# Performance work log

Hardware: AMD Instinct MI355X
Metric: run time of the kernel (lower is better)

Reference implementation:

```python
import jax, jax.numpy as jnp
import numpy as np

T, B, E, H, DFF, K = 1024, 4, 512, 8, 2048, 31
D = E // H  # head_dim


def double_swish(x):
    # DoubleSwish: x * sigmoid(x - 1)
    return x * jax.nn.sigmoid(x - 1.0)


def ffn(x, w1, b1, w2, b2):
    # ScaledLinear -> ActivationBalancer(identity in eval) -> DoubleSwish -> ScaledLinear
    return double_swish(x @ w1.T + b1) @ w2.T + b2


def rel_shift(x):
    # x: (B, H, T, 2T-1) -> (B, H, T, T); out[b,h,i,j] = x[b,h,i, (T-1) - i + j]
    t = x.shape[2]
    idx = (t - 1) - jnp.arange(t)[:, None] + jnp.arange(t)[None, :]  # (T, T)
    return jnp.take_along_axis(x, idx[None, None], axis=-1)


def self_attn(x, pos_emb, wqkv, bqkv, wo, bo, wpos, u, v):
    # x: (T, B, E); Transformer-XL style rel-pos multi-head attention
    t, b, e = x.shape
    qkv = x @ wqkv.T + bqkv                       # (T, B, 3E)
    q, k, val = jnp.split(qkv, 3, axis=-1)
    q = q * (D ** -0.5)
    to_heads = lambda z: z.reshape(t, b, H, D).transpose(1, 2, 0, 3)  # (B,H,T,D)
    q, k, val = to_heads(q), to_heads(k), to_heads(val)
    # positional projection: (1, 2T-1, E) -> (1, H, D, 2T-1)
    p = (pos_emb @ wpos.T).reshape(1, 2 * t - 1, H, D).transpose(0, 2, 3, 1)
    ac = jnp.einsum('bhld,bhsd->bhls', q + u[None, :, None, :], k)
    bd = jnp.einsum('bhld,bhdm->bhlm', q + v[None, :, None, :], p)
    scores = ac + rel_shift(bd)                   # (B, H, T, T)
    attn = jax.nn.softmax(scores, axis=-1)
    out = jnp.einsum('bhls,bhsd->bhld', attn, val)
    out = out.transpose(2, 0, 1, 3).reshape(t, b, e)  # (T, B, E)
    return out @ wo.T + bo


def conv_module(x, pw1_w, pw1_b, dw_w, dw_b, pw2_w, pw2_b):
    # x: (T, B, C) -> (B, C, T)
    x = x.transpose(1, 2, 0)
    x = jnp.einsum('oc,bct->bot', pw1_w, x) + pw1_b[None, :, None]  # (B, 2C, T)
    a, g = jnp.split(x, 2, axis=1)
    x = a * jax.nn.sigmoid(g)                     # GLU over channel dim
    pad = (K - 1) // 2
    x = jax.lax.conv_general_dilated(
        x, dw_w, window_strides=(1,), padding=[(pad, pad)],
        dimension_numbers=('NCH', 'OIH', 'NCH'), feature_group_count=E)
    x = double_swish(x + dw_b[None, :, None])
    x = jnp.einsum('oc,bct->bot', pw2_w, x) + pw2_b[None, :, None]
    return x.transpose(2, 0, 1)                   # (T, B, C)


def basic_norm(x, log_eps):
    # BasicNorm: x * (mean(x^2, -1) + exp(eps))^{-0.5}
    return x * jax.lax.rsqrt(jnp.mean(x * x, axis=-1, keepdims=True) + jnp.exp(log_eps))


def setup_inputs() -> dict:
    key = jax.random.key(0)
    ks = jax.random.split(key, 24)
    std = jnp.float32(0.02)
    f = lambda k, s: jax.random.normal(k, s, jnp.float32)
    return dict(
        src=f(ks[0], (T, B, E)),
        pos_emb=f(ks[1], (1, 2 * T - 1, E)),
        in_proj_w=f(ks[2], (3 * E, E)) * std,
        in_proj_b=f(ks[3], (3 * E,)) * std,
        out_proj_w=f(ks[4], (E, E)) * std,
        out_proj_b=f(ks[5], (E,)) * std,
        linear_pos_w=f(ks[6], (E, E)) * std,
        pos_bias_u=f(ks[7], (H, D)) * jnp.float32(0.01),
        pos_bias_v=f(ks[8], (H, D)) * jnp.float32(0.01),
        ffm_w1=f(ks[9], (DFF, E)) * std, ffm_b1=f(ks[10], (DFF,)) * std,
        ffm_w2=f(ks[11], (E, DFF)) * std, ffm_b2=f(ks[12], (E,)) * std,
        ff_w1=f(ks[13], (DFF, E)) * std, ff_b1=f(ks[14], (DFF,)) * std,
        ff_w2=f(ks[15], (E, DFF)) * std, ff_b2=f(ks[16], (E,)) * std,
        conv_pw1_w=f(ks[17], (2 * E, E)) * std, conv_pw1_b=f(ks[18], (2 * E,)) * std,
        conv_dw_w=f(ks[19], (E, 1, K)) * std, conv_dw_b=f(ks[20], (E,)) * std,
        conv_pw2_w=f(ks[21], (E, E)) * std, conv_pw2_b=f(ks[22], (E,)) * std,
        norm_eps=jnp.array(np.log(0.25), jnp.float32),
    )


def reference(src, pos_emb, in_proj_w, in_proj_b, out_proj_w, out_proj_b,
              linear_pos_w, pos_bias_u, pos_bias_v,
              ffm_w1, ffm_b1, ffm_w2, ffm_b2,
              ff_w1, ff_b1, ff_w2, ff_b2,
              conv_pw1_w, conv_pw1_b, conv_dw_w, conv_dw_b, conv_pw2_w, conv_pw2_b,
              norm_eps):
    # macaron FFN
    x = src + ffn(src, ffm_w1, ffm_b1, ffm_w2, ffm_b2)
    # rel-pos self-attention
    x = x + self_attn(x, pos_emb, in_proj_w, in_proj_b, out_proj_w, out_proj_b,
                      linear_pos_w, pos_bias_u, pos_bias_v)
    # convolution module
    x = x + conv_module(x, conv_pw1_w, conv_pw1_b, conv_dw_w, conv_dw_b, conv_pw2_w, conv_pw2_b)
    # second FFN
    x = x + ffn(x, ff_w1, ff_b1, ff_w2, ff_b2)
    # balancer is identity in eval; final BasicNorm
    return basic_norm(x, norm_eps)
```

## Files before the change

kernel.cpp:

```cpp
#include <hip/hip_runtime.h>
#include <string.h>


#define T_ 1024
#define B_ 4
#define E_ 512
#define H_ 8
#define DFF_ 2048
#define KW_ 31

typedef unsigned short u16;
typedef unsigned int u32;
typedef __bf16 bf16x8 __attribute__((ext_vector_type(8)));
typedef float floatx4 __attribute__((ext_vector_type(4)));

__device__ __forceinline__ float b2f(u16 u) {
    return __uint_as_float(((u32)u) << 16);
}
__device__ __forceinline__ u16 f2b(float f) {
    u32 i = __float_as_uint(f);
    u32 r = (i + 0x7fffu + ((i >> 16) & 1u)) >> 16;
    return (u16)r;
}

__device__ __forceinline__ void glds16(const u16 *g, u16 *l) {
    __builtin_amdgcn_global_load_lds((const __attribute__((address_space(1))) void *)g,
                                     (__attribute__((address_space(3))) void *)l, 16, 0, 0);
}

__global__ __launch_bounds__(256) void fill_k(float *out, long long n, float val) {
    long long g = (long long)blockIdx.x * 256 + threadIdx.x;
    if (g < n) out[g] = val;
}

__global__ __launch_bounds__(256) void detect_k(const u16 *src16, int *flag) {
    __shared__ int sh[256];
    int tid = threadIdx.x;
    int cnt = 0;
    for (int i = tid; i < 4096; i += 256) {
        u16 x = src16[2 * i];
        int e = (x >> 7) & 0xFF;
        cnt += (e == 0 || (e >= 0x70 && e <= 0x8F)) ? 1 : 0;
    }
    sh[tid] = cnt;
    __syncthreads();
    for (int s = 128; s; s >>= 1) {
        if (tid < s) sh[tid] += sh[tid + s];
        __syncthreads();
    }
    if (tid == 0) *flag = (sh[0] < 2048) ? 1 : 0;
}

struct CVT {
    const void *in[24];
    long long pre[25];
};

__global__ __launch_bounds__(256) void convert_k(CVT c, u16 *dst, const int *flag,
                                                 long long total) {
    long long g = (long long)blockIdx.x * 256 + threadIdx.x;
    if (g >= total) return;
    int s = 0;
#pragma unroll
    for (int i = 1; i < 25; i++) s += (g >= c.pre[i]) ? 1 : 0;
    long long l = g - c.pre[s];
    int f = *flag;
    u16 v = f ? f2b(((const float *)c.in[s])[l]) : ((const u16 *)c.in[s])[l];
    dst[g] = v;
}

struct GP {
    const u16 *A, *B;
    u16 *C;
    const u16 *bias;
    const void *resin;
    float *xr;
    u16 *xb;
    const u16 *ub, *vb;
    u16 *qu, *qv, *kh, *vt;
    int M, N, K, lda, ldb, ldc, mode, qcols, resin_f32;
    float qscale;
};

__global__ __launch_bounds__(512) void gemm_nt(GP p) {
    __shared__ __align__(16) u16 As[3 * 4096];
    __shared__ __align__(16) u16 Bs[3 * 4096];
    const int tid = threadIdx.x;
    const int wv = tid >> 6, ln = tid & 63;
    const int l16 = ln & 15, quad = ln >> 4;
    const int wm = (wv >> 2) << 5;
    const int wn = (wv & 3) << 4;
    const int gx = gridDim.x;
    const int nb = gx * gridDim.y;
    const int lid = blockIdx.y * gx + blockIdx.x;
    const int nid = (lid & 7) * (nb >> 3) + (lid >> 3);
    const int m0 = (nid / gx) << 6, n0 = (nid % gx) << 6;
    floatx4 zero = {0.f, 0.f, 0.f, 0.f};
    floatx4 acc[2];
    acc[0] = zero;
    acc[1] = zero;

    const int NT = p.K >> 6;

    const int srow = tid >> 3;
    const int sg = ((tid & 7) ^ (srow & 7)) << 3;
    int ra = m0 + srow;
    if (ra > p.M - 1) ra = p.M - 1;
    const u16 *Agp = p.A + (long long)ra * p.lda + sg;
    const u16 *Bgp = p.B + (long long)(n0 + srow) * p.ldb + sg;

    auto stage = [&](int bidx, int t) {
        const int k0 = t << 6;
        const int o = bidx << 12;
        glds16(Agp + k0, As + o + tid * 8);
        glds16(Bgp + k0, Bs + o + tid * 8);
    };

    stage(0, 0);
    stage(1, 1);
    stage(2, 2);
    asm volatile("s_waitcnt vmcnt(4)" ::: "memory");
    __builtin_amdgcn_s_barrier();

    int cb = 0;
    for (int t = 0; t < NT; t++) {
        const int o = cb << 12;
#pragma unroll
        for (int kk = 0; kk < 2; kk++) {
            const int swz = ((((kk << 2) | quad) ^ (l16 & 7)) << 3);
            bf16x8 bfv = __builtin_bit_cast(bf16x8,
                *(const uint4 *)&Bs[o + ((wn + l16) << 6) + swz]);
#pragma unroll
            for (int mt = 0; mt < 2; mt++) {
                bf16x8 af = __builtin_bit_cast(bf16x8,
                    *(const uint4 *)&As[o + ((wm + (mt << 4) + l16) << 6) + swz]);
                acc[mt] = __builtin_amdgcn_mfma_f32_16x16x32_bf16(af, bfv, acc[mt], 0, 0, 0);
            }
        }
        if (t + 1 < NT) {
            __builtin_amdgcn_sched_barrier(0);
            __builtin_amdgcn_s_barrier();
            if (t + 3 < NT) {
                stage(cb, t + 3);
                asm volatile("s_waitcnt vmcnt(4)" ::: "memory");
            } else if (t + 2 < NT) {
                asm volatile("s_waitcnt vmcnt(2)" ::: "memory");
            } else {
                asm volatile("s_waitcnt vmcnt(0)" ::: "memory");
            }
            __builtin_amdgcn_s_barrier();
            __builtin_amdgcn_sched_barrier(0);
        }
        cb = (cb == 2) ? 0 : cb + 1;
    }

#pragma unroll
    for (int mt = 0; mt < 2; mt++) {
#pragma unroll
        for (int r = 0; r < 4; r++) {
            int gr = m0 + wm + (mt << 4) + (quad << 2) + r;
            int gc = n0 + wn + l16;
            bool oob = gr >= p.M;
            if (oob && p.mode != 3) continue;
            float y = 0.f;
            if (!oob) {
                y = acc[mt][r];
                if (p.bias) y += b2f(p.bias[gc]);
                if (gc < p.qcols) y *= p.qscale;
            }
            if (p.mode == 3) {
                p.C[((gc >> 6) << 17) + (gr << 6) + (gc & 63)] = f2b(y);
            } else if (p.mode == 0) {
                p.C[(long long)gr * p.ldc + gc] = f2b(y);
            } else if (p.mode == 1) {
                float s = 1.f / (1.f + __expf(1.f - y));
                p.C[(long long)gr * p.ldc + gc] = f2b(y * s);
            } else {
                long long idx = (long long)gr * p.ldc + gc;
                float rv = p.resin_f32 ? ((const float *)p.resin)[idx]
                                       : b2f(((const u16 *)p.resin)[idx]);
                float o = rv + y;
                p.xr[idx] = o;
                if (p.xb) p.xb[idx] = f2b(o);
            }
        }
    }
}

__global__ __launch_bounds__(512) void gemm_nt128(GP p) {
    __shared__ __align__(16) u16 As[3 * 4096];
    __shared__ __align__(16) u16 Bs[3 * 4096];
    const int tid = threadIdx.x;
    const int wv = tid >> 6, ln = tid & 63;
    const int l16 = ln & 15, quad = ln >> 4;
    const int wm = (wv >> 2) << 6;
    const int wn = (wv & 3) << 5;
    const int gx = gridDim.x;
    const int nb = gx * gridDim.y;
    const int lid = blockIdx.y * gx + blockIdx.x;
    const int nid = (lid & 7) * (nb >> 3) + (lid >> 3);
    const int m0 = (nid / gx) << 7, n0 = (nid % gx) << 7;
    const int srow = tid >> 2;
    const int sg = ((tid & 3) ^ ((tid >> 3) & 3)) << 3;
    const u16 *Agp = p.A + (long long)(m0 + srow) * p.lda + sg;
    const u16 *Bgp = p.B + (long long)(n0 + srow) * p.ldb + sg;
    floatx4 zero = {0.f, 0.f, 0.f, 0.f};
    floatx4 acc[4][2];
#pragma unroll
    for (int i = 0; i < 4; i++)
#pragma unroll
        for (int j = 0; j < 2; j++) acc[i][j] = zero;

    const int rswz = ((quad ^ ((l16 >> 1) & 3)) << 3);
    const int NT = p.K >> 5;

    auto stage = [&](int bidx, int t) {
        const int k0 = t << 5;
        const int o = bidx << 12;
        glds16(Agp + k0, As + o + tid * 8);
        glds16(Bgp + k0, Bs + o + tid * 8);
    };

    stage(0, 0);
    stage(1, 1);
    stage(2, 2);
    asm volatile("s_waitcnt vmcnt(4)" ::: "memory");
    __builtin_amdgcn_s_barrier();

    int cb = 0;
    for (int t = 0; t < NT; t++) {
        const int o = cb << 12;
        bf16x8 av[4], bv[2];
#pragma unroll
        for (int mt = 0; mt < 4; mt++)
            av[mt] = __builtin_bit_cast(bf16x8,
                *(const uint4 *)&As[o + ((wm + (mt << 4) + l16) << 5) + rswz]);
#pragma unroll
        for (int nt = 0; nt < 2; nt++)
            bv[nt] = __builtin_bit_cast(bf16x8,
                *(const uint4 *)&Bs[o + ((wn + (nt << 4) + l16) << 5) + rswz]);
#pragma unroll
        for (int mt = 0; mt < 4; mt++)
#pragma unroll
            for (int nt = 0; nt < 2; nt++)
                acc[mt][nt] = __builtin_amdgcn_mfma_f32_16x16x32_bf16(av[mt], bv[nt],
                                                                      acc[mt][nt], 0, 0, 0);
        if (t + 1 < NT) {
            __builtin_amdgcn_sched_barrier(0);
            __builtin_amdgcn_s_barrier();
            if (t + 3 < NT) {
                stage(cb, t + 3);
                asm volatile("s_waitcnt vmcnt(4)" ::: "memory");
            } else if (t + 2 < NT) {
                asm volatile("s_waitcnt vmcnt(2)" ::: "memory");
            } else {
                asm volatile("s_waitcnt vmcnt(0)" ::: "memory");
            }
            __builtin_amdgcn_s_barrier();
            __builtin_amdgcn_sched_barrier(0);
        }
        cb = (cb == 2) ? 0 : cb + 1;
    }

#pragma unroll
    for (int mt = 0; mt < 4; mt++)
#pragma unroll
        for (int nt = 0; nt < 2; nt++)
#pragma unroll
            for (int r = 0; r < 4; r++) {
                int gr = m0 + wm + (mt << 4) + (quad << 2) + r;
                int gc = n0 + wn + (nt << 4) + l16;
                float y = acc[mt][nt][r];
                if (p.bias) y += b2f(p.bias[gc]);
                if (gc < p.qcols) y *= p.qscale;
                if (p.mode == 0) {
                    p.C[(long long)gr * p.ldc + gc] = f2b(y);
                } else if (p.mode == 1) {
                    float s = 1.f / (1.f + __expf(1.f - y));
                    p.C[(long long)gr * p.ldc + gc] = f2b(y * s);
                } else if (p.mode == 4) {
                    int t = gr >> 2, b = gr & 3;
                    if (gc < E_) {
                        int z = b * 8 + (gc >> 6);
                        long long oq = ((long long)z << 16) + (t << 6) + (gc & 63);
                        p.qu[oq] = f2b(y + b2f(p.ub[gc]));
                        p.qv[oq] = f2b(y + b2f(p.vb[gc]));
                    } else if (gc < 2 * E_) {
                        int c = gc - E_;
                        int z = b * 8 + (c >> 6);
                        p.kh[((long long)z << 16) + (t << 6) + (c & 63)] = f2b(y);
                    } else {
                        int c = gc - 2 * E_;
                        int z = b * 8 + (c >> 6);
                        p.vt[(long long)((z << 6) + (c & 63)) * T_ + t] = f2b(y);
                    }
                } else {
                    long long idx = (long long)gr * p.ldc + gc;
                    float rv = p.resin_f32 ? ((const float *)p.resin)[idx]
                                           : b2f(((const u16 *)p.resin)[idx]);
                    float o = rv + y;
                    p.xr[idx] = o;
                    if (p.xb) p.xb[idx] = f2b(o);
                }
            }
}

__global__ __launch_bounds__(256) void gemm_glu(const u16 *A, const u16 *W, const u16 *bias,
                                                u16 *ch) {
    __shared__ __align__(16) u16 As[3 * 4096];
    __shared__ __align__(16) u16 Ba[3 * 4096];
    __shared__ __align__(16) u16 Bg[3 * 4096];
    const int tid = threadIdx.x;
    const int wv = tid >> 6, ln = tid & 63;
    const int l16 = ln & 15, quad = ln >> 4;
    const int gx = gridDim.x;
    const int nb = gx * gridDim.y;
    const int lid = blockIdx.y * gx + blockIdx.x;
    const int nid = (lid & 7) * (nb >> 3) + (lid >> 3);
    const int m0 = (nid / gx) << 6, n0 = (nid % gx) << 6;
    floatx4 zero = {0.f, 0.f, 0.f, 0.f};
    floatx4 aa[4], ag[4];
#pragma unroll
    for (int i = 0; i < 4; i++) { aa[i] = zero; ag[i] = zero; }

    const int NT = 8;

    auto stage = [&](int bidx, int t) {
        const int k0 = t << 6;
        const int o = bidx << 12;
#pragma unroll
        for (int ps = 0; ps < 2; ps++) {
            int g = ps * 256 + tid;
            int row = g >> 3;
            int src = ((g & 7) ^ (row & 7)) << 3;
            glds16(A + ((m0 + row) << 9) + k0 + src, As + o + g * 8);
            glds16(W + ((n0 + row) << 9) + k0 + src, Ba + o + g * 8);
            glds16(W + ((E_ + n0 + row) << 9) + k0 + src, Bg + o + g * 8);
        }
    };

    stage(0, 0);
    stage(1, 1);
    stage(2, 2);
    asm volatile("s_waitcnt vmcnt(12)" ::: "memory");
    __builtin_amdgcn_s_barrier();

    int cb = 0;
    for (int t = 0; t < NT; t++) {
        const int o = cb << 12;
#pragma unroll
        for (int kk = 0; kk < 2; kk++) {
            const int swz = ((((kk << 2) | quad) ^ (l16 & 7)) << 3);
            bf16x8 af = __builtin_bit_cast(bf16x8,
                *(const uint4 *)&As[o + (((wv << 4) | l16) << 6) + swz]);
#pragma unroll
            for (int nt = 0; nt < 4; nt++) {
                bf16x8 bfa = __builtin_bit_cast(bf16x8,
                    *(const uint4 *)&Ba[o + (((nt << 4) | l16) << 6) + swz]);
                aa[nt] = __builtin_amdgcn_mfma_f32_16x16x32_bf16(af, bfa, aa[nt], 0, 0, 0);
                bf16x8 bfg = __builtin_bit_cast(bf16x8,
                    *(const uint4 *)&Bg[o + (((nt << 4) | l16) << 6) + swz]);
                ag[nt] = __builtin_amdgcn_mfma_f32_16x16x32_bf16(af, bfg, ag[nt], 0, 0, 0);
            }
        }
        if (t + 1 < NT) {
            __builtin_amdgcn_sched_barrier(0);
            __builtin_amdgcn_s_barrier();
            if (t + 3 < NT) {
                stage(cb, t + 3);
                asm volatile("s_waitcnt vmcnt(12)" ::: "memory");
            } else if (t + 2 < NT) {
                asm volatile("s_waitcnt vmcnt(6)" ::: "memory");
            } else {
                asm volatile("s_waitcnt vmcnt(0)" ::: "memory");
            }
            __builtin_amdgcn_s_barrier();
            __builtin_amdgcn_sched_barrier(0);
        }
        cb = (cb == 2) ? 0 : cb + 1;
    }

#pragma unroll
    for (int nt = 0; nt < 4; nt++) {
#pragma unroll
        for (int r = 0; r < 4; r++) {
            int gr = m0 + (wv << 4) + (quad << 2) + r;
            int gc = n0 + (nt << 4) + l16;
            float a = aa[nt][r] + b2f(bias[gc]);
            float g = ag[nt][r] + b2f(bias[E_ + gc]);
            ch[((long long)gr << 9) + gc] = f2b(a * (1.f / (1.f + __expf(-g))));
        }
    }
}

struct FK {
    const u16 *QU, *QV, *KH, *PPH, *VT;
    u16 *attno;
};

__global__ __launch_bounds__(256) void flash_k(FK p) {
    __shared__ __align__(16) u16 lds[2 * 16384 + 4608];

    const int tid = threadIdx.x;
    const int wv = tid >> 6, ln = tid & 63;
    const int l16 = ln & 15, quad = ln >> 4;
    const int lid = blockIdx.y * 16 + blockIdx.x;
    const int nid = (lid & 7) * 64 + (lid >> 3);
    const int zg = nid >> 4;
    const int i0 = (nid & 15) << 6;
    const u16 *kh0 = p.KH + (long long)zg * 65536;
    const u16 *ph0 = p.PPH + (long long)(zg & 7) * 131072;
    const u16 *vt0 = p.VT + (long long)zg * 65536;
    u16 *Pb = lds + 32768;

    auto stage = [&](int buf, int jt) {
        const int j0 = jt << 6;
        const int m_start = 960 - i0 + j0;
        u16 *Kh = lds + (buf << 14);
        u16 *Vt = Kh + 4096;
        u16 *Ph = Kh + 8192;
#pragma unroll
        for (int ps = 0; ps < 2; ps++) {
            int g = ps * 256 + tid;
            int row = g >> 3;
            int src = ((g & 7) ^ (row & 7)) << 3;
            glds16(kh0 + ((j0 + row) << 6) + src, Kh + g * 8);
            glds16(vt0 + (row << 10) + j0 + src, Vt + g * 8);
        }
#pragma unroll
        for (int ps = 0; ps < 4; ps++) {
            int g = ps * 256 + tid;
            int row = g >> 3;
            int src = ((g & 7) ^ (row & 7)) << 3;
            glds16(ph0 + ((m_start + row) << 6) + src, Ph + g * 8);
        }
    };

    const long long qoff = (long long)zg * 65536 + (long long)(i0 + (wv << 4) + l16) * 64 + (quad << 3);
    bf16x8 aqu[2], aqv[2];
#pragma unroll
    for (int kk = 0; kk < 2; kk++) {
        aqu[kk] = __builtin_bit_cast(bf16x8, *(const uint4 *)(p.QU + qoff + (kk << 5)));
        aqv[kk] = __builtin_bit_cast(bf16x8, *(const uint4 *)(p.QV + qoff + (kk << 5)));
    }

    stage(0, 0);
    asm volatile("s_waitcnt vmcnt(0)" ::: "memory");
    __builtin_amdgcn_s_barrier();

    float lacc[4];
    floatx4 accO[4];
    floatx4 zero = {0.f, 0.f, 0.f, 0.f};
#pragma unroll
    for (int e = 0; e < 4; e++) lacc[e] = 0.f;
#pragma unroll
    for (int i = 0; i < 4; i++) accO[i] = zero;

    const int r16q = quad << 2;

    for (int jt = 0; jt < 16; jt++) {
        if (jt + 1 < 16) stage((jt + 1) & 1, jt + 1);
        __builtin_amdgcn_sched_barrier(0);
        const int o = (jt & 1) << 14;
        const u16 *Kh = lds + o;
        const u16 *Vt = lds + o + 4096;
        const u16 *Ph = lds + o + 8192;

        floatx4 aS[4], aB[5];
#pragma unroll
        for (int i = 0; i < 4; i++) aS[i] = zero;
#pragma unroll
        for (int i = 0; i < 5; i++) aB[i] = zero;
        __builtin_amdgcn_s_setprio(1);
#pragma unroll
        for (int kk = 0; kk < 2; kk++) {
            const int swz = ((((kk << 2) | quad) ^ (l16 & 7)) << 3);
#pragma unroll
            for (int nt = 0; nt < 4; nt++) {
                bf16x8 bf = __builtin_bit_cast(bf16x8,
                    *(const uint4 *)&Kh[(((nt << 4) | l16) << 6) + swz]);
                aS[nt] = __builtin_amdgcn_mfma_f32_16x16x32_bf16(aqu[kk], bf, aS[nt], 0, 0, 0);
            }
#pragma unroll
            for (int rt = 0; rt < 5; rt++) {
                bf16x8 bf = __builtin_bit_cast(bf16x8,
                    *(const uint4 *)&Ph[((((rt + 3 - wv) << 4) | l16) << 6) + swz]);
                aB[rt] = __builtin_amdgcn_mfma_f32_16x16x32_bf16(aqv[kk], bf, aB[rt], 0, 0, 0);
            }
        }
        __builtin_amdgcn_s_setprio(0);

#pragma unroll
        for (int e = 0; e < 4; e++) {
            const int r16 = r16q + e;
            const int t = l16 + 15 - r16;
            const int srcl = (quad << 4) | (t & 15);
            const int carry = t >> 4;
            float ps = 0.f;
#pragma unroll
            for (int nt = 0; nt < 4; nt++) {
                float vlo = __shfl(aB[nt][e], srcl, 64);
                float vhi = __shfl(aB[nt + 1][e], srcl, 64);
                float bd = carry ? vhi : vlo;
                float pe = __expf(aS[nt][e] + bd);
                ps += pe;
                Pb[(((wv << 4) + r16) * 72) + (nt << 4) + l16] = f2b(pe);
            }
            lacc[e] += ps;
        }

        __builtin_amdgcn_s_setprio(1);
#pragma unroll
        for (int kk = 0; kk < 2; kk++) {
            const int swz = ((((kk << 2) | quad) ^ (l16 & 7)) << 3);
            bf16x8 ap = __builtin_bit_cast(bf16x8,
                *(const uint4 *)&Pb[(((wv << 4) | l16) * 72) + (kk << 5) + (quad << 3)]);
#pragma unroll
            for (int nd = 0; nd < 4; nd++) {
                bf16x8 bv = __builtin_bit_cast(bf16x8,
                    *(const uint4 *)&Vt[(((nd << 4) | l16) << 6) + swz]);
                accO[nd] = __builtin_amdgcn_mfma_f32_16x16x32_bf16(ap, bv, accO[nd], 0, 0, 0);
            }
        }
        __builtin_amdgcn_s_setprio(0);

        if (jt + 1 < 16) {
            __builtin_amdgcn_sched_barrier(0);
            __builtin_amdgcn_s_barrier();
            asm volatile("s_waitcnt vmcnt(0)" ::: "memory");
            __builtin_amdgcn_s_barrier();
            __builtin_amdgcn_sched_barrier(0);
        }
    }

    const int b = zg >> 3, h = zg & 7;
#pragma unroll
    for (int e = 0; e < 4; e++) {
#pragma unroll
        for (int msk = 1; msk < 16; msk <<= 1) lacc[e] += __shfl_xor(lacc[e], msk, 64);
        float inv = 1.f / lacc[e];
        int t = i0 + (wv << 4) + (quad << 2) + e;
#pragma unroll
        for (int nd = 0; nd < 4; nd++) {
            int d = (nd << 4) + l16;
            p.attno[(long long)(t * B_ + b) * E_ + h * 64 + d] = f2b(accO[nd][e] * inv);
        }
    }
}


__global__ __launch_bounds__(256) void dwconv_k(const u16 *ch, const u16 *w, const u16 *bias,
                                                u16 *cd) {
    const int cp = threadIdx.x;
    const int b = blockIdx.x >> 7;
    const int t0 = (blockIdx.x & 127) << 3;
    const int c0 = cp << 1;
    float in0[38], in1[38];
#pragma unroll
    for (int j = 0; j < 38; j++) {
        int tt = t0 - 15 + j;
        u32 v = 0;
        if (tt >= 0 && tt < T_) v = *(const u32 *)&ch[tt * 2048 + b * 512 + c0];
        in0[j] = b2f((u16)(v & 0xffff));
        in1[j] = b2f((u16)(v >> 16));
    }
    float w0[KW_], w1[KW_];
#pragma unroll
    for (int kk = 0; kk < KW_; kk++) {
        w0[kk] = b2f(w[c0 * KW_ + kk]);
        w1[kk] = b2f(w[c0 * KW_ + KW_ + kk]);
    }
    float bi0 = b2f(bias[c0]), bi1 = b2f(bias[c0 + 1]);
#pragma unroll
    for (int t = 0; t < 8; t++) {
        float a0 = bi0, a1 = bi1;
#pragma unroll
        for (int kk = 0; kk < KW_; kk++) {
            a0 += in0[t + kk] * w0[kk];
            a1 += in1[t + kk] * w1[kk];
        }
        float s0 = 1.f / (1.f + __expf(1.f - a0));
        float s1 = 1.f / (1.f + __expf(1.f - a1));
        u32 o = (u32)f2b(a0 * s0) | ((u32)f2b(a1 * s1) << 16);
        *(u32 *)&cd[(t0 + t) * 2048 + b * 512 + c0] = o;
    }
}

__global__ __launch_bounds__(256) void norm_k(const float *xr, const float *epsp, float *out) {
    int wv = threadIdx.x >> 6, ln = threadIdx.x & 63;
    long long row = blockIdx.x * 4 + wv;
    const float *x = xr + row * E_;
    float vals[8], ss = 0.f;
#pragma unroll
    for (int i = 0; i < 8; i++) {
        vals[i] = x[ln + (i << 6)];
        ss += vals[i] * vals[i];
    }
#pragma unroll
    for (int m = 32; m; m >>= 1) ss += __shfl_xor(ss, m, 64);
    float sc = rsqrtf(ss * (1.f / (float)E_) + __expf(epsp[0]));
    float *o = out + row * E_;
#pragma unroll
    for (int i = 0; i < 8; i++) o[ln + (i << 6)] = vals[i] * sc;
}


extern "C" void kernel_launch(void *const *d_in, const int *in_sizes, int n_in,
                              void *d_out, int out_size, void *d_ws, size_t ws_size,
                              hipStream_t stream) {
    const size_t MB = (size_t)1 << 20;
    static const long long EXPECT[24] = {
        2097152, 1048064, 786432, 1536, 262144, 512, 262144, 512, 512,
        1048576, 2048, 1048576, 512, 1048576, 2048, 1048576, 512,
        524288, 1024, 15872, 512, 262144, 512, 1};
    const size_t NEED = 93 * MB;

    float code = 0.f;
    if (n_in != 24) {
        code = 1000.f + (float)n_in;
    } else {
        for (int i = 0; i < 24; i++) {
            if ((long long)in_sizes[i] != EXPECT[i]) { code = 2000.f + 64.f * i; break; }
        }
    }
    if (code == 0.f && out_size != 2097152) code = 3000.f;
    if (code == 0.f && ws_size < NEED) code = 5000.f + (float)(ws_size / MB);
    if (code != 0.f) {
        long long n = (long long)out_size;
        fill_k<<<dim3((unsigned)((n + 255) / 256)), dim3(256), 0, stream>>>((float *)d_out, n, code);
        return;
    }

    char *w = (char *)d_ws;
    int *flag = (int *)(w + 0);
    u16 *cv = (u16 *)(w + 1 * MB);
    float *xr = (float *)(w + 21 * MB);
    u16 *xb = (u16 *)(w + 29 * MB);
    u16 *h1 = (u16 *)(w + 33 * MB);
    u16 *pph = (u16 *)(w + 63 * MB);
    u16 *QU = (u16 *)(w + 65 * MB);
    u16 *QV = (u16 *)(w + 69 * MB);
    u16 *KH = (u16 *)(w + 73 * MB);
    u16 *VT = (u16 *)(w + 77 * MB);
    u16 *attno = (u16 *)(w + 81 * MB);
    u16 *ch = (u16 *)(w + 85 * MB);
    u16 *cd = (u16 *)(w + 89 * MB);

    detect_k<<<dim3(1), dim3(256), 0, stream>>>((const u16 *)d_in[0], flag);
    CVT c;
    c.pre[0] = 0;
    for (int i = 0; i < 24; i++) {
        c.in[i] = d_in[i];
        c.pre[i + 1] = c.pre[i] + in_sizes[i];
    }
    long long total = c.pre[24];
    convert_k<<<dim3((unsigned)((total + 255) / 256)), dim3(256), 0, stream>>>(c, cv, flag, total);

    const u16 *src = cv + c.pre[0];
    const u16 *pos_emb = cv + c.pre[1];
    const u16 *w_qkv = cv + c.pre[2];
    const u16 *b_qkv = cv + c.pre[3];
    const u16 *w_o = cv + c.pre[4];
    const u16 *b_o = cv + c.pre[5];
    const u16 *w_pos = cv + c.pre[6];
    const u16 *u_bias = cv + c.pre[7];
    const u16 *v_bias = cv + c.pre[8];
    const u16 *ffm_w1 = cv + c.pre[9];
    const u16 *ffm_b1 = cv + c.pre[10];
    const u16 *ffm_w2 = cv + c.pre[11];
    const u16 *ffm_b2 = cv + c.pre[12];
    const u16 *ff_w1 = cv + c.pre[13];
    const u16 *ff_b1 = cv + c.pre[14];
    const u16 *ff_w2 = cv + c.pre[15];
    const u16 *ff_b2 = cv + c.pre[16];
    const u16 *pw1_w = cv + c.pre[17];
    const u16 *pw1_b = cv + c.pre[18];
    const u16 *dw_w = cv + c.pre[19];
    const u16 *dw_b = cv + c.pre[20];
    const u16 *pw2_w = cv + c.pre[21];
    const u16 *pw2_b = cv + c.pre[22];

    auto mk = [](const void *A, int lda, const void *B, int ldb, void *C, int ldc,
                 const void *bias, int M, int N, int K, int mode) {
        GP p;
        memset(&p, 0, sizeof(p));
        p.A = (const u16 *)A; p.B = (const u16 *)B; p.C = (u16 *)C; p.bias = (const u16 *)bias;
        p.M = M; p.N = N; p.K = K; p.lda = lda; p.ldb = ldb; p.ldc = ldc; p.mode = mode;
        p.qscale = 1.f;
        return p;
    };
    auto launch = [&](GP p) {
        dim3 g((p.N + 63) / 64, (p.M + 63) / 64, 1);
        gemm_nt<<<g, dim3(512), 0, stream>>>(p);
    };
    auto launch128 = [&](GP p) {
        dim3 g(p.N >> 7, p.M >> 7, 1);
        gemm_nt128<<<g, dim3(512), 0, stream>>>(p);
    };

    const int M = T_ * B_;

    { GP p = mk(src, E_, ffm_w1, E_, h1, DFF_, ffm_b1, M, DFF_, E_, 1); launch128(p); }
    { GP p = mk(h1, DFF_, ffm_w2, DFF_, nullptr, E_, ffm_b2, M, E_, DFF_, 2);
      p.resin = d_in[0]; p.resin_f32 = 1; p.xr = xr; p.xb = xb; launch(p); }

    { GP p = mk(xb, E_, w_qkv, E_, nullptr, 3 * E_, b_qkv, M, 3 * E_, E_, 4);
      p.qcols = E_; p.qscale = 0.125f;
      p.ub = u_bias; p.vb = v_bias; p.qu = QU; p.qv = QV; p.kh = KH; p.vt = VT;
      launch128(p); }
    { GP p = mk(pos_emb, E_, w_pos, E_, pph, E_, nullptr, 2 * T_ - 1, E_, E_, 3); launch(p); }

    {
        FK f;
        f.QU = QU; f.QV = QV; f.KH = KH; f.PPH = pph; f.VT = VT; f.attno = attno;
        flash_k<<<dim3(16, 32), dim3(256), 0, stream>>>(f);
    }

    { GP p = mk(attno, E_, w_o, E_, nullptr, E_, b_o, M, E_, E_, 2);
      p.resin = xr; p.resin_f32 = 1; p.xr = xr; p.xb = xb; launch(p); }

    gemm_glu<<<dim3(8, 64), dim3(256), 0, stream>>>(xb, pw1_w, pw1_b, ch);
    dwconv_k<<<dim3(512), dim3(256), 0, stream>>>(ch, dw_w, dw_b, cd);
    { GP p = mk(cd, E_, pw2_w, E_, nullptr, E_, pw2_b, M, E_, E_, 2);
      p.resin = xr; p.resin_f32 = 1; p.xr = xr; p.xb = xb; launch(p); }

    { GP p = mk(xb, E_, ff_w1, E_, h1, DFF_, ff_b1, M, DFF_, E_, 1); launch128(p); }
    { GP p = mk(h1, DFF_, ff_w2, DFF_, nullptr, E_, ff_b2, M, E_, DFF_, 2);
      p.resin = xr; p.resin_f32 = 1; p.xr = xr; p.xb = nullptr; launch(p); }

    norm_k<<<dim3(M / 4), dim3(256), 0, stream>>>(xr, (const float *)d_in[23], (float *)d_out);
}
```

Measured before the change: 366.3 us.

## Use 8 waves in GLU GEMM and single-buffer K/P in flash attention

The GLU pointwise GEMM now runs 512 threads per block, and each wave computes a 32x16 sub-tile instead of 16x64. Staging becomes one load per operand per thread, with the vmcnt waits adjusted to match. In the flash attention kernel, K and positional tiles become single-buffered while V stays double-buffered. The next K/P/V prefetch is issued right after the score MFMAs behind a barrier, and the B-D shuffles are hoisted so five shuffles replace eight. The aim is lower LDS use for higher occupancy and more waves to hide latency, at the cost of an extra barrier inside the loop.

```diff
diff --git a/kernel.cpp b/kernel.cpp
--- a/kernel.cpp
+++ b/kernel.cpp
@@ -305,7 +305,7 @@
             }
 }
 
-__global__ __launch_bounds__(256) void gemm_glu(const u16 *A, const u16 *W, const u16 *bias,
+__global__ __launch_bounds__(512) void gemm_glu(const u16 *A, const u16 *W, const u16 *bias,
                                                 u16 *ch) {
     __shared__ __align__(16) u16 As[3 * 4096];
     __shared__ __align__(16) u16 Ba[3 * 4096];
@@ -313,36 +313,36 @@
     const int tid = threadIdx.x;
     const int wv = tid >> 6, ln = tid & 63;
     const int l16 = ln & 15, quad = ln >> 4;
+    const int wm = (wv >> 2) << 5;
+    const int wn = (wv & 3) << 4;
     const int gx = gridDim.x;
     const int nb = gx * gridDim.y;
     const int lid = blockIdx.y * gx + blockIdx.x;
     const int nid = (lid & 7) * (nb >> 3) + (lid >> 3);
     const int m0 = (nid / gx) << 6, n0 = (nid % gx) << 6;
     floatx4 zero = {0.f, 0.f, 0.f, 0.f};
-    floatx4 aa[4], ag[4];
-#pragma unroll
-    for (int i = 0; i < 4; i++) { aa[i] = zero; ag[i] = zero; }
+    floatx4 aa[2], ag[2];
+    aa[0] = zero; aa[1] = zero; ag[0] = zero; ag[1] = zero;
 
     const int NT = 8;
+    const int srow = tid >> 3;
+    const int sg = ((tid & 7) ^ (srow & 7)) << 3;
+    const u16 *Agp = A + ((long long)(m0 + srow) << 9) + sg;
+    const u16 *Bap = W + ((long long)(n0 + srow) << 9) + sg;
+    const u16 *Bgp = W + ((long long)(E_ + n0 + srow) << 9) + sg;
 
     auto stage = [&](int bidx, int t) {
         const int k0 = t << 6;
         const int o = bidx << 12;
-#pragma unroll
-        for (int ps = 0; ps < 2; ps++) {
-            int g = ps * 256 + tid;
-            int row = g >> 3;
-            int src = ((g & 7) ^ (row & 7)) << 3;
-            glds16(A + ((m0 + row) << 9) + k0 + src, As + o + g * 8);
-            glds16(W + ((n0 + row) << 9) + k0 + src, Ba + o + g * 8);
-            glds16(W + ((E_ + n0 + row) << 9) + k0 + src, Bg + o + g * 8);
-        }
+        glds16(Agp + k0, As + o + tid * 8);
+        glds16(Bap + k0, Ba + o + tid * 8);
+        glds16(Bgp + k0, Bg + o + tid * 8);
     };
 
     stage(0, 0);
     stage(1, 1);
     stage(2, 2);
-    asm volatile("s_waitcnt vmcnt(12)" ::: "memory");
+    asm volatile("s_waitcnt vmcnt(6)" ::: "memory");
     __builtin_amdgcn_s_barrier();
 
     int cb = 0;
@@ -351,16 +351,16 @@
 #pragma unroll
         for (int kk = 0; kk < 2; kk++) {
             const int swz = ((((kk << 2) | quad) ^ (l16 & 7)) << 3);
-            bf16x8 af = __builtin_bit_cast(bf16x8,
-                *(const uint4 *)&As[o + (((wv << 4) | l16) << 6) + swz]);
-#pragma unroll
-            for (int nt = 0; nt < 4; nt++) {
-                bf16x8 bfa = __builtin_bit_cast(bf16x8,
-                    *(const uint4 *)&Ba[o + (((nt << 4) | l16) << 6) + swz]);
-                aa[nt] = __builtin_amdgcn_mfma_f32_16x16x32_bf16(af, bfa, aa[nt], 0, 0, 0);
-                bf16x8 bfg = __builtin_bit_cast(bf16x8,
-                    *(const uint4 *)&Bg[o + (((nt << 4) | l16) << 6) + swz]);
-                ag[nt] = __builtin_amdgcn_mfma_f32_16x16x32_bf16(af, bfg, ag[nt], 0, 0, 0);
+            bf16x8 ba = __builtin_bit_cast(bf16x8,
+                *(const uint4 *)&Ba[o + ((wn + l16) << 6) + swz]);
+            bf16x8 bg = __builtin_bit_cast(bf16x8,
+                *(const uint4 *)&Bg[o + ((wn + l16) << 6) + swz]);
+#pragma unroll
+            for (int mt = 0; mt < 2; mt++) {
+                bf16x8 af = __builtin_bit_cast(bf16x8,
+                    *(const uint4 *)&As[o + ((wm + (mt << 4) + l16) << 6) + swz]);
+                aa[mt] = __builtin_amdgcn_mfma_f32_16x16x32_bf16(af, ba, aa[mt], 0, 0, 0);
+                ag[mt] = __builtin_amdgcn_mfma_f32_16x16x32_bf16(af, bg, ag[mt], 0, 0, 0);
             }
         }
         if (t + 1 < NT) {
@@ -368,9 +368,9 @@
             __builtin_amdgcn_s_barrier();
             if (t + 3 < NT) {
                 stage(cb, t + 3);
-                asm volatile("s_waitcnt vmcnt(12)" ::: "memory");
+                asm volatile("s_waitcnt vmcnt(6)" ::: "memory");
             } else if (t + 2 < NT) {
-                asm volatile("s_waitcnt vmcnt(6)" ::: "memory");
+                asm volatile("s_waitcnt vmcnt(3)" ::: "memory");
             } else {
                 asm volatile("s_waitcnt vmcnt(0)" ::: "memory");
             }
@@ -381,13 +381,13 @@
     }
 
 #pragma unroll
-    for (int nt = 0; nt < 4; nt++) {
+    for (int mt = 0; mt < 2; mt++) {
 #pragma unroll
         for (int r = 0; r < 4; r++) {
-            int gr = m0 + (wv << 4) + (quad << 2) + r;
-            int gc = n0 + (nt << 4) + l16;
-            float a = aa[nt][r] + b2f(bias[gc]);
-            float g = ag[nt][r] + b2f(bias[E_ + gc]);
+            int gr = m0 + wm + (mt << 4) + (quad << 2) + r;
+            int gc = n0 + wn + l16;
+            float a = aa[mt][r] + b2f(bias[gc]);
+            float g = ag[mt][r] + b2f(bias[E_ + gc]);
             ch[((long long)gr << 9) + gc] = f2b(a * (1.f / (1.f + __expf(-g))));
         }
     }
@@ -399,7 +399,10 @@
 };
 
 __global__ __launch_bounds__(256) void flash_k(FK p) {
-    __shared__ __align__(16) u16 lds[2 * 16384 + 4608];
+    __shared__ __align__(16) u16 lds[25088];
+    u16 *Kh = lds;
+    u16 *Ph = lds + 4096;
+    u16 *Pb = lds + 20480;
 
     const int tid = threadIdx.x;
     const int wv = tid >> 6, ln = tid & 63;
@@ -411,21 +414,16 @@
     const u16 *kh0 = p.KH + (long long)zg * 65536;
     const u16 *ph0 = p.PPH + (long long)(zg & 7) * 131072;
     const u16 *vt0 = p.VT + (long long)zg * 65536;
-    u16 *Pb = lds + 32768;
-
-    auto stage = [&](int buf, int jt) {
+
+    auto stage_kp = [&](int jt) {
         const int j0 = jt << 6;
         const int m_start = 960 - i0 + j0;
-        u16 *Kh = lds + (buf << 14);
-        u16 *Vt = Kh + 4096;
-        u16 *Ph = Kh + 8192;
 #pragma unroll
         for (int ps = 0; ps < 2; ps++) {
             int g = ps * 256 + tid;
             int row = g >> 3;
             int src = ((g & 7) ^ (row & 7)) << 3;
             glds16(kh0 + ((j0 + row) << 6) + src, Kh + g * 8);
-            glds16(vt0 + (row << 10) + j0 + src, Vt + g * 8);
         }
 #pragma unroll
         for (int ps = 0; ps < 4; ps++) {
@@ -435,6 +433,17 @@
             glds16(ph0 + ((m_start + row) << 6) + src, Ph + g * 8);
         }
     };
+    auto stage_v = [&](int buf, int jt) {
+        const int j0 = jt << 6;
+        u16 *Vt = lds + 12288 + (buf << 12);
+#pragma unroll
+        for (int ps = 0; ps < 2; ps++) {
+            int g = ps * 256 + tid;
+            int row = g >> 3;
+            int src = ((g & 7) ^ (row & 7)) << 3;
+            glds16(vt0 + (row << 10) + j0 + src, Vt + g * 8);
+        }
+    };
 
     const long long qoff = (long long)zg * 65536 + (long long)(i0 + (wv << 4) + l16) * 64 + (quad << 3);
     bf16x8 aqu[2], aqv[2];
@@ -444,7 +453,8 @@
         aqv[kk] = __builtin_bit_cast(bf16x8, *(const uint4 *)(p.QV + qoff + (kk << 5)));
     }
 
-    stage(0, 0);
+    stage_kp(0);
+    stage_v(0, 0);
     asm volatile("s_waitcnt vmcnt(0)" ::: "memory");
     __builtin_amdgcn_s_barrier();
 
@@ -459,13 +469,6 @@
     const int r16q = quad << 2;
 
     for (int jt = 0; jt < 16; jt++) {
-        if (jt + 1 < 16) stage((jt + 1) & 1, jt + 1);
-        __builtin_amdgcn_sched_barrier(0);
-        const int o = (jt & 1) << 14;
-        const u16 *Kh = lds + o;
-        const u16 *Vt = lds + o + 4096;
-        const u16 *Ph = lds + o + 8192;
-
         floatx4 aS[4], aB[5];
 #pragma unroll
         for (int i = 0; i < 4; i++) aS[i] = zero;
@@ -489,6 +492,13 @@
             }
         }
         __builtin_amdgcn_s_setprio(0);
+        __builtin_amdgcn_sched_barrier(0);
+        __builtin_amdgcn_s_barrier();
+        if (jt + 1 < 16) {
+            stage_kp(jt + 1);
+            stage_v((jt + 1) & 1, jt + 1);
+        }
+        __builtin_amdgcn_sched_barrier(0);
 
 #pragma unroll
         for (int e = 0; e < 4; e++) {
@@ -496,12 +506,13 @@
             const int t = l16 + 15 - r16;
             const int srcl = (quad << 4) | (t & 15);
             const int carry = t >> 4;
+            float s5[5];
+#pragma unroll
+            for (int rt = 0; rt < 5; rt++) s5[rt] = __shfl(aB[rt][e], srcl, 64);
             float ps = 0.f;
 #pragma unroll
             for (int nt = 0; nt < 4; nt++) {
-                float vlo = __shfl(aB[nt][e], srcl, 64);
-                float vhi = __shfl(aB[nt + 1][e], srcl, 64);
-                float bd = carry ? vhi : vlo;
+                float bd = carry ? s5[nt + 1] : s5[nt];
                 float pe = __expf(aS[nt][e] + bd);
                 ps += pe;
                 Pb[(((wv << 4) + r16) * 72) + (nt << 4) + l16] = f2b(pe);
@@ -509,6 +520,7 @@
             lacc[e] += ps;
         }
 
+        const u16 *Vt = lds + 12288 + ((jt & 1) << 12);
         __builtin_amdgcn_s_setprio(1);
 #pragma unroll
         for (int kk = 0; kk < 2; kk++) {
@@ -526,7 +538,6 @@
 
         if (jt + 1 < 16) {
             __builtin_amdgcn_sched_barrier(0);
-            __builtin_amdgcn_s_barrier();
             asm volatile("s_waitcnt vmcnt(0)" ::: "memory");
             __builtin_amdgcn_s_barrier();
             __builtin_amdgcn_sched_barrier(0);
@@ -719,7 +730,7 @@
     { GP p = mk(attno, E_, w_o, E_, nullptr, E_, b_o, M, E_, E_, 2);
       p.resin = xr; p.resin_f32 = 1; p.xr = xr; p.xb = xb; launch(p); }
 
-    gemm_glu<<<dim3(8, 64), dim3(256), 0, stream>>>(xb, pw1_w, pw1_b, ch);
+    gemm_glu<<<dim3(8, 64), dim3(512), 0, stream>>>(xb, pw1_w, pw1_b, ch);
     dwconv_k<<<dim3(512), dim3(256), 0, stream>>>(ch, dw_w, dw_b, cd);
     { GP p = mk(cd, E_, pw2_w, E_, nullptr, E_, pw2_b, M, E_, E_, 2);
       p.resin = xr; p.resin_f32 = 1; p.xr = xr; p.xb = xb; launch(p); }
```

Result: no change. 373.1 us (+1.9%).
